# Optimization experiments

Hardware: AMD Instinct MI355X
Metric: run time of the kernel (lower is better)

The kernel has to match this reference:

```python
import jax, jax.numpy as jnp
import numpy as np

E = 2048      # embed_dim
HQ = 16       # query heads
HK = 4        # kv heads
D = E // HQ   # head_dim = 128
G = HQ // HK  # head groups = 4
KVE = D * HK  # kv_embed_dim = 512
B, N = 2, 2048


def setup_inputs() -> dict:
    key = jax.random.key(0)
    ks = jax.random.split(key, 8)
    s_q = (2.0 / (E + E)) ** 0.5      # xavier_normal for square proj
    s_kv = (2.0 / (E + KVE)) ** 0.5   # xavier_normal for kv proj
    return {
        "query": jax.random.normal(ks[0], (B, N, E), jnp.float32),
        "key":   jax.random.normal(ks[1], (B, N, E), jnp.float32),
        "value": jax.random.normal(ks[2], (B, N, E), jnp.float32),
        "Wq": jax.random.normal(ks[3], (E, E), jnp.float32) * s_q,
        "bq_": jnp.zeros((E,), jnp.float32),
        "Wk": jax.random.normal(ks[4], (KVE, E), jnp.float32) * s_kv,
        "bk_": jnp.zeros((KVE,), jnp.float32),
        "Wv": jax.random.normal(ks[5], (KVE, E), jnp.float32) * s_kv,
        "bv_": jnp.zeros((KVE,), jnp.float32),
        "Wo": jax.random.normal(ks[6], (E, E), jnp.float32) * s_q,
        "bo_": jnp.zeros((E,), jnp.float32),
        "is_causal": 1,
    }


def reference(query, key, value, Wq, bq_, Wk, bk_, Wv, bv_, Wo, bo_, is_causal):
    b, n, _ = query.shape
    s = key.shape[1]
    # projections (torch Linear: y = x @ W.T + b)
    q = (query @ Wq.T + bq_).reshape(b, n, HQ, D).transpose(0, 2, 1, 3)  # b hq n d
    k = (key   @ Wk.T + bk_).reshape(b, s, HK, D).transpose(0, 2, 1, 3)  # b hk s d
    v = (value @ Wv.T + bv_).reshape(b, s, HK, D).transpose(0, 2, 1, 3)  # b hk s d
    q = q / (D ** 0.5)
    # split query heads 'b (h g) n d -> b g h n d' (h = kv heads outer, g inner)
    qg = q.reshape(b, HK, G, n, D).transpose(0, 2, 1, 3, 4)              # b g h n d
    sim = jnp.einsum('bghnd,bhsd->bghns', qg, k)                          # b g h n s
    if is_causal:
        causal = jnp.tril(jnp.ones((n, s), dtype=bool))
        sim = jnp.where(causal, sim, jnp.finfo(sim.dtype).min)
    attn = jax.nn.softmax(sim, axis=-1)
    out = jnp.einsum('bghns,bhsd->bghnd', attn, v)                        # b g h n d
    # 'b g h n d -> b n (h g) d' then merge heads
    out = out.transpose(0, 3, 2, 1, 4).reshape(b, n, E)
    return out @ Wo.T + bo_
```

## Files before the change

### kernel.cpp

```cpp
#include <hip/hip_runtime.h>
#include <stdint.h>

#define E_   2048
#define HQ_  16
#define HK_  4
#define D_   128
#define G_   4
#define KVE_ 512
#define B_   2
#define N_   2048
#define MTOT (B_*N_)

#define QSC 0.12751743f

typedef __attribute__((ext_vector_type(8))) short bf16x8;
typedef __attribute__((ext_vector_type(4))) float f32x4;

__device__ __forceinline__ unsigned short f2bf(float f) {
  union { float f; uint32_t u; } a; a.f = f;
  uint32_t u = a.u;
  uint32_t r = (u + 0x7fffu + ((u >> 16) & 1u)) >> 16;
  return (unsigned short)r;
}

__device__ __forceinline__ uint32_t pack_bf2(float a, float b) {
  union { float f; uint32_t u; } x, y; x.f = a; y.f = b;
  return (x.u >> 16) | (y.u & 0xffff0000u);
}

__device__ __forceinline__ void g2l16(const void* g, void* l) {
  __builtin_amdgcn_global_load_lds(
      (__attribute__((address_space(1))) void*)(void*)(uintptr_t)g,
      (__attribute__((address_space(3))) void*)l,
      16, 0, 0);
}

__global__ void cast_all(const float* __restrict__ q, const float* __restrict__ k,
                         const float* __restrict__ v, const float* __restrict__ wq,
                         const float* __restrict__ wk, const float* __restrict__ wv,
                         const float* __restrict__ wo, unsigned short* __restrict__ dst) {
  int i = blockIdx.x * 256 + threadIdx.x;
  const float* src; int base;
  if      (i < 2097152) { src = q;  base = 0; }
  else if (i < 4194304) { src = k;  base = 2097152; }
  else if (i < 6291456) { src = v;  base = 4194304; }
  else if (i < 7340032) { src = wq; base = 6291456; }
  else if (i < 7602176) { src = wk; base = 7340032; }
  else if (i < 7864320) { src = wv; base = 7602176; }
  else                  { src = wo; base = 7864320; }
  float4 val = ((const float4*)src)[i - base];
  ushort4 o;
  o.x = f2bf(val.x); o.y = f2bf(val.y); o.z = f2bf(val.z); o.w = f2bf(val.w);
  ((ushort4*)dst)[i] = o;
}

__device__ __forceinline__ void gemm_kloop(const unsigned short* __restrict__ A,
                                           const unsigned short* __restrict__ W,
                                           unsigned short* As, unsigned short* Bs,
                                           int bm, int bn, int K,
                                           int wm, int wn, int tid, int l16, int quad,
                                           f32x4 acc[4][4]) {
  for (int k0 = 0; k0 < K; k0 += 32) {
    __syncthreads();
#pragma unroll
    for (int r = 0; r < 2; ++r) {
      int c = r * 256 + tid;
      int row = c >> 2, c8 = (c & 3) << 3;
      g2l16(A + (size_t)(bm + row) * K + k0 + c8, (char*)As + (size_t)c * 16);
    }
#pragma unroll
    for (int r = 0; r < 2; ++r) {
      int c = r * 256 + tid;
      int row = c >> 2, c8 = (c & 3) << 3;
      g2l16(W + (size_t)(bn + row) * K + k0 + c8, (char*)Bs + (size_t)c * 16);
    }
    __syncthreads();

    bf16x8 af[4], bf[4];
#pragma unroll
    for (int mi = 0; mi < 4; ++mi)
      af[mi] = *(const bf16x8*)(As + (wm + mi * 16 + l16) * 32 + quad * 8);
#pragma unroll
    for (int ni = 0; ni < 4; ++ni)
      bf[ni] = *(const bf16x8*)(Bs + (wn + ni * 16 + l16) * 32 + quad * 8);
#pragma unroll
    for (int mi = 0; mi < 4; ++mi)
#pragma unroll
      for (int ni = 0; ni < 4; ++ni)
        acc[mi][ni] = __builtin_amdgcn_mfma_f32_16x16x32_bf16(af[mi], bf[ni], acc[mi][ni], 0, 0, 0);
  }
}

__global__ __launch_bounds__(256, 2)
void proj_fused(const unsigned short* __restrict__ qb, const unsigned short* __restrict__ kb,
                const unsigned short* __restrict__ vb,
                const unsigned short* __restrict__ Wqb, const unsigned short* __restrict__ Wkb,
                const unsigned short* __restrict__ Wvb,
                const float* __restrict__ bq, const float* __restrict__ bk,
                const float* __restrict__ bv,
                unsigned short* __restrict__ Qb, unsigned short* __restrict__ Kpp,
                unsigned short* __restrict__ Vtt) {
  __shared__ unsigned short As[128 * 32];
  __shared__ unsigned short Bs[128 * 32];
  const int tid  = threadIdx.x;
  const int wave = tid >> 6, lane = tid & 63;
  const int l16  = lane & 15, quad = lane >> 4;
  const int bm = blockIdx.x * 128;
  const int wm = (wave & 1) * 64, wn = (wave >> 1) * 64;
  const int y = blockIdx.y;

  const unsigned short *A, *W;
  const float* bias;
  unsigned short* out;
  int bn, mode, Nn;
  float scale;
  if (y < 16)      { A = qb; W = Wqb; bias = bq; out = Qb;  bn = y * 128;        mode = 0; Nn = 2048; scale = QSC;  }
  else if (y < 20) { A = kb; W = Wkb; bias = bk; out = Kpp; bn = (y - 16) * 128; mode = 0; Nn = 512;  scale = 1.0f; }
  else             { A = vb; W = Wvb; bias = bv; out = Vtt; bn = (y - 20) * 128; mode = 1; Nn = 512;  scale = 1.0f; }

  f32x4 acc[4][4] = {};
  gemm_kloop(A, W, As, Bs, bm, bn, E_, wm, wn, tid, l16, quad, acc);

  if (mode == 0) {
#pragma unroll
    for (int mi = 0; mi < 4; ++mi)
#pragma unroll
      for (int ni = 0; ni < 4; ++ni) {
        int col = bn + wn + ni * 16 + l16;
        float bb = bias[col];
        int row0 = bm + wm + mi * 16 + quad * 4;
#pragma unroll
        for (int r = 0; r < 4; ++r)
          out[(size_t)(row0 + r) * Nn + col] = f2bf((acc[mi][ni][r] + bb) * scale);
      }
  } else {
#pragma unroll
    for (int mi = 0; mi < 4; ++mi)
#pragma unroll
      for (int ni = 0; ni < 4; ++ni) {
        int col = bn + wn + ni * 16 + l16;
        float bb = bias[col];
        int row0 = bm + wm + mi * 16 + quad * 4;
        int b = row0 >> 11, s = row0 & 2047;
        ushort4 o;
        o.x = f2bf(acc[mi][ni][0] + bb);
        o.y = f2bf(acc[mi][ni][1] + bb);
        o.z = f2bf(acc[mi][ni][2] + bb);
        o.w = f2bf(acc[mi][ni][3] + bb);
        *(ushort4*)(out + (size_t)(b * KVE_ + col) * N_ + s) = o;
      }
  }
}

__global__ __launch_bounds__(256, 2)
void gemm_out(const unsigned short* __restrict__ A, const unsigned short* __restrict__ W,
              const float* __restrict__ bias, float* __restrict__ Cout) {
  __shared__ unsigned short As[128 * 32];
  __shared__ unsigned short Bs[128 * 32];
  const int tid  = threadIdx.x;
  const int wave = tid >> 6, lane = tid & 63;
  const int l16  = lane & 15, quad = lane >> 4;
  const int bm = blockIdx.x * 128, bn = blockIdx.y * 128;
  const int wm = (wave & 1) * 64, wn = (wave >> 1) * 64;

  f32x4 acc[4][4] = {};
  gemm_kloop(A, W, As, Bs, bm, bn, E_, wm, wn, tid, l16, quad, acc);

#pragma unroll
  for (int mi = 0; mi < 4; ++mi)
#pragma unroll
    for (int ni = 0; ni < 4; ++ni) {
      int col = bn + wn + ni * 16 + l16;
      float bb = bias[col];
      int row0 = bm + wm + mi * 16 + quad * 4;
#pragma unroll
      for (int r = 0; r < 4; ++r)
        Cout[(size_t)(row0 + r) * E_ + col] = acc[mi][ni][r] + bb;
    }
}

__global__ __launch_bounds__(256, 2)
void attn_gqa(const unsigned short* __restrict__ Qp,
              const unsigned short* __restrict__ Kp,
              const unsigned short* __restrict__ Vt,
              unsigned short* __restrict__ Ob,
              const int* __restrict__ is_causal_p) {
  __shared__ unsigned short lds[2][16384];

  const int tid  = threadIdx.x;
  const int wave = tid >> 6, lane = tid & 63;
  const int l16  = lane & 15, quad = lane >> 4;
  const int qg = wave >> 1, sg = wave & 1;
  const int p = blockIdx.x, bh = blockIdx.y;
  const int b = bh >> 4, hq = bh & 15, hk = hq >> 2;
  const int causal = *is_causal_p;

  const unsigned short* Kbase = Kp + (size_t)b * N_ * KVE_ + hk * D_;
  const unsigned short* Vbase = Vt + (size_t)(b * KVE_ + hk * D_) * N_;

  auto stage = [&](int t, int buf) {
    int s0 = t * 64;
    unsigned short* Kd = &lds[buf][0];
    unsigned short* Vd = &lds[buf][8192];
#pragma unroll
    for (int r = 0; r < 4; ++r) {
      int idx = r * 256 + tid;
      int s = (idx >> 8) * 16 + (idx & 15);
      int d = ((idx >> 6) & 3) * 32 + ((idx >> 4) & 3) * 8;
      g2l16(Kbase + (size_t)(s0 + s) * KVE_ + d, Kd + (size_t)idx * 8);
    }
#pragma unroll
    for (int r = 0; r < 4; ++r) {
      int idx = r * 256 + tid;
      int d = (idx >> 7) * 16 + (idx & 15);
      int sc = ((idx >> 6) & 1) * 32 + ((idx >> 4) & 3) * 8;
      g2l16(Vbase + (size_t)d * N_ + s0 + sc, Vd + (size_t)idx * 8);
    }
  };

  for (int half = 0; half < 2; ++half) {
    const int qt = half ? (31 - p) : p;
    const int nt = causal ? qt + 1 : (N_ / 64);
    const int qw = qt * 64 + qg * 32;

    bf16x8 qf[2][4];
#pragma unroll
    for (int mi = 0; mi < 2; ++mi)
#pragma unroll
      for (int kk = 0; kk < 4; ++kk)
        qf[mi][kk] = *(const bf16x8*)(Qp + (size_t)(b * N_ + qw + mi * 16 + l16) * E_ +
                                      hq * D_ + kk * 32 + quad * 8);

    f32x4 o[2][8] = {};
    float tsum[2] = { 0.f, 0.f };

    stage(0, 0);
    __syncthreads();

    for (int t = 0; t < nt; ++t) {
      if (t + 1 < nt) stage(t + 1, (t + 1) & 1);
      const unsigned short* Kb = &lds[t & 1][0];
      const unsigned short* Vb = &lds[t & 1][8192];
      const int sw = t * 64 + sg * 32;
      const bool active = !causal || (sw <= qw + 31);

      if (active) {
        f32x4 sa[2][2] = {};
#pragma unroll
        for (int kk = 0; kk < 4; ++kk) {
          bf16x8 kf[2];
#pragma unroll
          for (int ni = 0; ni < 2; ++ni)
            kf[ni] = *(const bf16x8*)(Kb + (((sg * 2 + ni) * 4 + kk) * 64 + lane) * 8);
#pragma unroll
          for (int mi = 0; mi < 2; ++mi)
#pragma unroll
            for (int ni = 0; ni < 2; ++ni)
              sa[mi][ni] = __builtin_amdgcn_mfma_f32_16x16x32_bf16(kf[ni], qf[mi][kk], sa[mi][ni], 0, 0, 0);
        }

        if (causal && sw + 31 > qw) {
#pragma unroll
          for (int mi = 0; mi < 2; ++mi)
#pragma unroll
            for (int ni = 0; ni < 2; ++ni) {
              int sbase = sw + ni * 16 + quad * 4;
              int q = qw + mi * 16 + l16;
#pragma unroll
              for (int r = 0; r < 4; ++r)
                if (sbase + r > q) sa[mi][ni][r] = -3.0e38f;
            }
        }

        uint32_t pk[2][2][2];
#pragma unroll
        for (int mi = 0; mi < 2; ++mi)
#pragma unroll
          for (int ni = 0; ni < 2; ++ni) {
#pragma unroll
            for (int r = 0; r < 4; ++r) {
              float e = __builtin_amdgcn_exp2f(sa[mi][ni][r]);
              tsum[mi] += e;
              sa[mi][ni][r] = e;
            }
            pk[mi][ni][0] = pack_bf2(sa[mi][ni][0], sa[mi][ni][1]);
            pk[mi][ni][1] = pack_bf2(sa[mi][ni][2], sa[mi][ni][3]);
          }

        bf16x8 vf[8];
#pragma unroll
        for (int n8 = 0; n8 < 8; ++n8)
          vf[n8] = *(const bf16x8*)(Vb + ((n8 * 2 + sg) * 64 + lane) * 8);
#pragma unroll
        for (int mi = 0; mi < 2; ++mi) {
          union { bf16x8 v; uint32_t u[4]; } pb;
#pragma unroll
          for (int h = 0; h < 4; ++h) {
            int src = ((quad & 1) * 2 + (h >> 1)) * 16 + l16;
            uint32_t v0 = __shfl(pk[mi][0][h & 1], src);
            uint32_t v1 = __shfl(pk[mi][1][h & 1], src);
            pb.u[h] = (quad & 2) ? v1 : v0;
          }
#pragma unroll
          for (int n8 = 0; n8 < 8; ++n8)
            o[mi][n8] = __builtin_amdgcn_mfma_f32_16x16x32_bf16(vf[n8], pb.v, o[mi][n8], 0, 0, 0);
        }
      }
      __syncthreads();
    }

    float4* X4 = (float4*)&lds[0][0];
    float*  Xt = (float*)&lds[0][0] + 8192;
    if (sg == 1) {
#pragma unroll
      for (int mi = 0; mi < 2; ++mi) {
#pragma unroll
        for (int ni = 0; ni < 8; ++ni) {
          float4 w;
          w.x = o[mi][ni][0]; w.y = o[mi][ni][1]; w.z = o[mi][ni][2]; w.w = o[mi][ni][3];
          X4[((qg * 2 + mi) * 8 + ni) * 64 + lane] = w;
        }
        Xt[(qg * 2 + mi) * 64 + lane] = tsum[mi];
      }
    }
    __syncthreads();
    if (sg == 0) {
#pragma unroll
      for (int mi = 0; mi < 2; ++mi) {
        float lt = tsum[mi] + Xt[(qg * 2 + mi) * 64 + lane];
        lt += __shfl_xor(lt, 16);
        lt += __shfl_xor(lt, 32);
        float inv = 1.0f / lt;
        int q = qw + mi * 16 + l16;
#pragma unroll
        for (int ni = 0; ni < 8; ++ni) {
          float4 xx = X4[((qg * 2 + mi) * 8 + ni) * 64 + lane];
          ushort4 st;
          st.x = f2bf((o[mi][ni][0] + xx.x) * inv);
          st.y = f2bf((o[mi][ni][1] + xx.y) * inv);
          st.z = f2bf((o[mi][ni][2] + xx.z) * inv);
          st.w = f2bf((o[mi][ni][3] + xx.w) * inv);
          *(ushort4*)(Ob + (size_t)(b * N_ + q) * E_ + hq * D_ + ni * 16 + quad * 4) = st;
        }
      }
    }
    __syncthreads();
  }
}

extern "C" void kernel_launch(void* const* d_in, const int* in_sizes, int n_in,
                              void* d_out, int out_size, void* d_ws, size_t ws_size,
                              hipStream_t stream) {
  const float* query = (const float*)d_in[0];
  const float* key   = (const float*)d_in[1];
  const float* value = (const float*)d_in[2];
  const float* Wq = (const float*)d_in[3];
  const float* bq = (const float*)d_in[4];
  const float* Wk = (const float*)d_in[5];
  const float* bk = (const float*)d_in[6];
  const float* Wv = (const float*)d_in[7];
  const float* bv = (const float*)d_in[8];
  const float* Wo = (const float*)d_in[9];
  const float* bo = (const float*)d_in[10];
  const int* is_causal = (const int*)d_in[11];

  char* ws = (char*)d_ws;
  size_t off = 0;
  auto alloc = [&](size_t bytes) {
    char* p = ws + off;
    off += (bytes + 255) & ~(size_t)255;
    return p;
  };
  unsigned short* qb  = (unsigned short*)alloc((size_t)MTOT * E_ * 2);
  unsigned short* kb  = (unsigned short*)alloc((size_t)MTOT * E_ * 2);
  unsigned short* vb  = (unsigned short*)alloc((size_t)MTOT * E_ * 2);
  unsigned short* Wqb = (unsigned short*)alloc((size_t)E_ * E_ * 2);
  unsigned short* Wkb = (unsigned short*)alloc((size_t)KVE_ * E_ * 2);
  unsigned short* Wvb = (unsigned short*)alloc((size_t)KVE_ * E_ * 2);
  unsigned short* Wob = (unsigned short*)alloc((size_t)E_ * E_ * 2);
  unsigned short* Qb  = (unsigned short*)alloc((size_t)MTOT * E_ * 2);
  unsigned short* Kpp = (unsigned short*)alloc((size_t)MTOT * KVE_ * 2);
  unsigned short* Vtt = (unsigned short*)alloc((size_t)MTOT * KVE_ * 2);
  unsigned short* Ob  = (unsigned short*)alloc((size_t)MTOT * E_ * 2);
  (void)ws_size; (void)n_in; (void)in_sizes; (void)out_size;

  dim3 blk(256);
  cast_all<<<dim3(34816), blk, 0, stream>>>(query, key, value, Wq, Wk, Wv, Wo, qb);
  proj_fused<<<dim3(32, 24), blk, 0, stream>>>(qb, kb, vb, Wqb, Wkb, Wvb,
                                               bq, bk, bv, Qb, Kpp, Vtt);
  attn_gqa<<<dim3(16, 32), blk, 0, stream>>>(Qb, Kpp, Vtt, Ob, is_causal);
  gemm_out<<<dim3(32, 16), blk, 0, stream>>>(Ob, Wob, bo, (float*)d_out);
}
```

Before: 360.7 us.

## Restructure GQA attention to one q-tile per block with 32-wide KV tiles

Attention blocks now process a single 64-row query tile, with each wave owning 16 query rows across the full key range, removing the key-split and its LDS reduction. KV tiles shrink to 32 keys, halving LDS so more blocks fit per CU; the grid doubles and q-tiles are assigned with a rotated mapping to balance causal work. Projection kernel launch bounds are also raised. This trades lower K/V reuse per block and more barriers per unit of work for higher occupancy and simpler epilogue.

```diff
diff --git a/kernel.cpp b/kernel.cpp
--- a/kernel.cpp
+++ b/kernel.cpp
@@ -91,7 +91,7 @@
   }
 }
 
-__global__ __launch_bounds__(256, 2)
+__global__ __launch_bounds__(256, 3)
 void proj_fused(const unsigned short* __restrict__ qb, const unsigned short* __restrict__ kb,
                 const unsigned short* __restrict__ vb,
                 const unsigned short* __restrict__ Wqb, const unsigned short* __restrict__ Wkb,
@@ -179,172 +179,135 @@
     }
 }
 
-__global__ __launch_bounds__(256, 2)
+__global__ __launch_bounds__(256, 4)
 void attn_gqa(const unsigned short* __restrict__ Qp,
               const unsigned short* __restrict__ Kp,
               const unsigned short* __restrict__ Vt,
               unsigned short* __restrict__ Ob,
               const int* __restrict__ is_causal_p) {
-  __shared__ unsigned short lds[2][16384];
+  __shared__ unsigned short lds[2][8192];
 
   const int tid  = threadIdx.x;
   const int wave = tid >> 6, lane = tid & 63;
   const int l16  = lane & 15, quad = lane >> 4;
-  const int qg = wave >> 1, sg = wave & 1;
-  const int p = blockIdx.x, bh = blockIdx.y;
+  const int bh = blockIdx.y;
+  const int u  = (blockIdx.x + bh) & 31;
+  const int qt = (u < 16) ? u : 47 - u;
   const int b = bh >> 4, hq = bh & 15, hk = hq >> 2;
   const int causal = *is_causal_p;
 
   const unsigned short* Kbase = Kp + (size_t)b * N_ * KVE_ + hk * D_;
   const unsigned short* Vbase = Vt + (size_t)(b * KVE_ + hk * D_) * N_;
 
+  const int nt = causal ? 2 * qt + 2 : (N_ / 32);
+  const int qw = qt * 64 + wave * 16;
+
   auto stage = [&](int t, int buf) {
-    int s0 = t * 64;
+    int s0 = t * 32;
     unsigned short* Kd = &lds[buf][0];
-    unsigned short* Vd = &lds[buf][8192];
-#pragma unroll
-    for (int r = 0; r < 4; ++r) {
+    unsigned short* Vd = &lds[buf][4096];
+#pragma unroll
+    for (int r = 0; r < 2; ++r) {
       int idx = r * 256 + tid;
       int s = (idx >> 8) * 16 + (idx & 15);
       int d = ((idx >> 6) & 3) * 32 + ((idx >> 4) & 3) * 8;
       g2l16(Kbase + (size_t)(s0 + s) * KVE_ + d, Kd + (size_t)idx * 8);
     }
 #pragma unroll
-    for (int r = 0; r < 4; ++r) {
+    for (int r = 0; r < 2; ++r) {
       int idx = r * 256 + tid;
-      int d = (idx >> 7) * 16 + (idx & 15);
-      int sc = ((idx >> 6) & 1) * 32 + ((idx >> 4) & 3) * 8;
+      int d = (idx >> 6) * 16 + (idx & 15);
+      int sc = ((idx >> 4) & 3) * 8;
       g2l16(Vbase + (size_t)d * N_ + s0 + sc, Vd + (size_t)idx * 8);
     }
   };
 
-  for (int half = 0; half < 2; ++half) {
-    const int qt = half ? (31 - p) : p;
-    const int nt = causal ? qt + 1 : (N_ / 64);
-    const int qw = qt * 64 + qg * 32;
-
-    bf16x8 qf[2][4];
-#pragma unroll
-    for (int mi = 0; mi < 2; ++mi)
-#pragma unroll
-      for (int kk = 0; kk < 4; ++kk)
-        qf[mi][kk] = *(const bf16x8*)(Qp + (size_t)(b * N_ + qw + mi * 16 + l16) * E_ +
-                                      hq * D_ + kk * 32 + quad * 8);
-
-    f32x4 o[2][8] = {};
-    float tsum[2] = { 0.f, 0.f };
-
-    stage(0, 0);
+  bf16x8 qf[4];
+#pragma unroll
+  for (int kk = 0; kk < 4; ++kk)
+    qf[kk] = *(const bf16x8*)(Qp + (size_t)(b * N_ + qw + l16) * E_ +
+                              hq * D_ + kk * 32 + quad * 8);
+
+  f32x4 o[8] = {};
+  float tsum = 0.f;
+
+  stage(0, 0);
+  __syncthreads();
+
+  for (int t = 0; t < nt; ++t) {
+    if (t + 1 < nt) stage(t + 1, (t + 1) & 1);
+    const unsigned short* Kb = &lds[t & 1][0];
+    const unsigned short* Vb = &lds[t & 1][4096];
+    const int sw = t * 32;
+    const bool active = !causal || (sw <= qw + 15);
+
+    if (active) {
+      f32x4 sa[2] = {};
+#pragma unroll
+      for (int kk = 0; kk < 4; ++kk) {
+        bf16x8 kf0 = *(const bf16x8*)(Kb + ((kk)     * 64 + lane) * 8);
+        bf16x8 kf1 = *(const bf16x8*)(Kb + ((4 + kk) * 64 + lane) * 8);
+        sa[0] = __builtin_amdgcn_mfma_f32_16x16x32_bf16(kf0, qf[kk], sa[0], 0, 0, 0);
+        sa[1] = __builtin_amdgcn_mfma_f32_16x16x32_bf16(kf1, qf[kk], sa[1], 0, 0, 0);
+      }
+
+      if (causal && sw + 31 > qw) {
+        int q = qw + l16;
+#pragma unroll
+        for (int ni = 0; ni < 2; ++ni) {
+          int sbase = sw + ni * 16 + quad * 4;
+#pragma unroll
+          for (int r = 0; r < 4; ++r)
+            if (sbase + r > q) sa[ni][r] = -3.0e38f;
+        }
+      }
+
+      uint32_t pk[2][2];
+#pragma unroll
+      for (int ni = 0; ni < 2; ++ni) {
+#pragma unroll
+        for (int r = 0; r < 4; ++r) {
+          float e = __builtin_amdgcn_exp2f(sa[ni][r]);
+          tsum += e;
+          sa[ni][r] = e;
+        }
+        pk[ni][0] = pack_bf2(sa[ni][0], sa[ni][1]);
+        pk[ni][1] = pack_bf2(sa[ni][2], sa[ni][3]);
+      }
+
+      union { bf16x8 v; uint32_t w[4]; } pb;
+#pragma unroll
+      for (int h = 0; h < 4; ++h) {
+        int src = ((quad & 1) * 2 + (h >> 1)) * 16 + l16;
+        uint32_t v0 = __shfl(pk[0][h & 1], src);
+        uint32_t v1 = __shfl(pk[1][h & 1], src);
+        pb.w[h] = (quad & 2) ? v1 : v0;
+      }
+
+      bf16x8 vf[8];
+#pragma unroll
+      for (int n8 = 0; n8 < 8; ++n8)
+        vf[n8] = *(const bf16x8*)(Vb + (n8 * 64 + lane) * 8);
+#pragma unroll
+      for (int n8 = 0; n8 < 8; ++n8)
+        o[n8] = __builtin_amdgcn_mfma_f32_16x16x32_bf16(vf[n8], pb.v, o[n8], 0, 0, 0);
+    }
     __syncthreads();
-
-    for (int t = 0; t < nt; ++t) {
-      if (t + 1 < nt) stage(t + 1, (t + 1) & 1);
-      const unsigned short* Kb = &lds[t & 1][0];
-      const unsigned short* Vb = &lds[t & 1][8192];
-      const int sw = t * 64 + sg * 32;
-      const bool active = !causal || (sw <= qw + 31);
-
-      if (active) {
-        f32x4 sa[2][2] = {};
-#pragma unroll
-        for (int kk = 0; kk < 4; ++kk) {
-          bf16x8 kf[2];
-#pragma unroll
-          for (int ni = 0; ni < 2; ++ni)
-            kf[ni] = *(const bf16x8*)(Kb + (((sg * 2 + ni) * 4 + kk) * 64 + lane) * 8);
-#pragma unroll
-          for (int mi = 0; mi < 2; ++mi)
-#pragma unroll
-            for (int ni = 0; ni < 2; ++ni)
-              sa[mi][ni] = __builtin_amdgcn_mfma_f32_16x16x32_bf16(kf[ni], qf[mi][kk], sa[mi][ni], 0, 0, 0);
-        }
-
-        if (causal && sw + 31 > qw) {
-#pragma unroll
-          for (int mi = 0; mi < 2; ++mi)
-#pragma unroll
-            for (int ni = 0; ni < 2; ++ni) {
-              int sbase = sw + ni * 16 + quad * 4;
-              int q = qw + mi * 16 + l16;
-#pragma unroll
-              for (int r = 0; r < 4; ++r)
-                if (sbase + r > q) sa[mi][ni][r] = -3.0e38f;
-            }
-        }
-
-        uint32_t pk[2][2][2];
-#pragma unroll
-        for (int mi = 0; mi < 2; ++mi)
-#pragma unroll
-          for (int ni = 0; ni < 2; ++ni) {
-#pragma unroll
-            for (int r = 0; r < 4; ++r) {
-              float e = __builtin_amdgcn_exp2f(sa[mi][ni][r]);
-              tsum[mi] += e;
-              sa[mi][ni][r] = e;
-            }
-            pk[mi][ni][0] = pack_bf2(sa[mi][ni][0], sa[mi][ni][1]);
-            pk[mi][ni][1] = pack_bf2(sa[mi][ni][2], sa[mi][ni][3]);
-          }
-
-        bf16x8 vf[8];
-#pragma unroll
-        for (int n8 = 0; n8 < 8; ++n8)
-          vf[n8] = *(const bf16x8*)(Vb + ((n8 * 2 + sg) * 64 + lane) * 8);
-#pragma unroll
-        for (int mi = 0; mi < 2; ++mi) {
-          union { bf16x8 v; uint32_t u[4]; } pb;
-#pragma unroll
-          for (int h = 0; h < 4; ++h) {
-            int src = ((quad & 1) * 2 + (h >> 1)) * 16 + l16;
-            uint32_t v0 = __shfl(pk[mi][0][h & 1], src);
-            uint32_t v1 = __shfl(pk[mi][1][h & 1], src);
-            pb.u[h] = (quad & 2) ? v1 : v0;
-          }
-#pragma unroll
-          for (int n8 = 0; n8 < 8; ++n8)
-            o[mi][n8] = __builtin_amdgcn_mfma_f32_16x16x32_bf16(vf[n8], pb.v, o[mi][n8], 0, 0, 0);
-        }
-      }
-      __syncthreads();
-    }
-
-    float4* X4 = (float4*)&lds[0][0];
-    float*  Xt = (float*)&lds[0][0] + 8192;
-    if (sg == 1) {
-#pragma unroll
-      for (int mi = 0; mi < 2; ++mi) {
-#pragma unroll
-        for (int ni = 0; ni < 8; ++ni) {
-          float4 w;
-          w.x = o[mi][ni][0]; w.y = o[mi][ni][1]; w.z = o[mi][ni][2]; w.w = o[mi][ni][3];
-          X4[((qg * 2 + mi) * 8 + ni) * 64 + lane] = w;
-        }
-        Xt[(qg * 2 + mi) * 64 + lane] = tsum[mi];
-      }
-    }
-    __syncthreads();
-    if (sg == 0) {
-#pragma unroll
-      for (int mi = 0; mi < 2; ++mi) {
-        float lt = tsum[mi] + Xt[(qg * 2 + mi) * 64 + lane];
-        lt += __shfl_xor(lt, 16);
-        lt += __shfl_xor(lt, 32);
-        float inv = 1.0f / lt;
-        int q = qw + mi * 16 + l16;
-#pragma unroll
-        for (int ni = 0; ni < 8; ++ni) {
-          float4 xx = X4[((qg * 2 + mi) * 8 + ni) * 64 + lane];
-          ushort4 st;
-          st.x = f2bf((o[mi][ni][0] + xx.x) * inv);
-          st.y = f2bf((o[mi][ni][1] + xx.y) * inv);
-          st.z = f2bf((o[mi][ni][2] + xx.z) * inv);
-          st.w = f2bf((o[mi][ni][3] + xx.w) * inv);
-          *(ushort4*)(Ob + (size_t)(b * N_ + q) * E_ + hq * D_ + ni * 16 + quad * 4) = st;
-        }
-      }
-    }
-    __syncthreads();
+  }
+
+  float lt = tsum;
+  lt += __shfl_xor(lt, 16);
+  lt += __shfl_xor(lt, 32);
+  float inv = 1.0f / lt;
+  int q = qw + l16;
+#pragma unroll
+  for (int n8 = 0; n8 < 8; ++n8) {
+    ushort4 st;
+    st.x = f2bf(o[n8][0] * inv);
+    st.y = f2bf(o[n8][1] * inv);
+    st.z = f2bf(o[n8][2] * inv);
+    st.w = f2bf(o[n8][3] * inv);
+    *(ushort4*)(Ob + (size_t)(b * N_ + q) * E_ + hq * D_ + n8 * 16 + quad * 4) = st;
   }
 }
 
@@ -388,6 +351,6 @@
   cast_all<<<dim3(34816), blk, 0, stream>>>(query, key, value, Wq, Wk, Wv, Wo, qb);
   proj_fused<<<dim3(32, 24), blk, 0, stream>>>(qb, kb, vb, Wqb, Wkb, Wvb,
                                                bq, bk, bv, Qb, Kpp, Vtt);
-  attn_gqa<<<dim3(16, 32), blk, 0, stream>>>(Qb, Kpp, Vtt, Ob, is_causal);
+  attn_gqa<<<dim3(32, 32), blk, 0, stream>>>(Qb, Kpp, Vtt, Ob, is_causal);
   gemm_out<<<dim3(32, 16), blk, 0, stream>>>(Ob, Wob, bo, (float*)d_out);
 }
```

After: 360.0 us. No clear change (-0.2%).
